# Kernel optimization log

Hardware: AMD Instinct MI355X
Metric: run time of the kernel (lower is better)

Reference implementation:

```python
import jax, jax.numpy as jnp
import numpy as np

# Dims: batch B, seq S, model dim D (= embedding_size = input_size of every block
# since hidden_size == embedding_size), sLSTM hidden H.
B, S, D, H = 8, 1024, 1024, 1024
NBLOCKS = 2
EPS = 1e-5  # nn.LayerNorm default


def _xavier(key, shape):
    fan_out, fan_in = shape
    lim = float(np.sqrt(6.0 / (fan_in + fan_out)))
    return jax.random.uniform(key, shape, jnp.float32, -lim, lim)


def setup_inputs() -> dict:
    key = jax.random.key(0)
    ks = jax.random.split(key, 1 + NBLOCKS * 4)
    inp = {"input_seq": jax.random.normal(ks[0], (B, S, D), jnp.float32)}
    for i in range(NBLOCKS):
        din = D  # every block has input_size == hidden_size == 1024
        k = ks[1 + 4 * i: 1 + 4 * (i + 1)]
        # fused gate weights, gate order [i, f, z, o]
        inp[f"W{i}"] = _xavier(k[0], (4 * H, din))      # input->gates
        inp[f"R{i}"] = _xavier(k[1], (4 * H, H))        # recurrent h->gates
        inp[f"b{i}"] = jnp.zeros((4 * H,), jnp.float32)
        inp[f"projW{i}"] = _xavier(k[2], (din, H))      # block output proj (xavier, zero bias per reset_parameters)
        inp[f"projb{i}"] = jnp.zeros((din,), jnp.float32)
        inp[f"gamma{i}"] = jnp.ones((din,), jnp.float32)   # LayerNorm weight
        inp[f"beta{i}"] = jnp.zeros((din,), jnp.float32)   # LayerNorm bias
    return inp


def _slstm(x, W, R, b):
    """Exponential-gated, log-stabilized sLSTM scan. x: (B,S,Din) -> (B,S,H)."""
    Hh = R.shape[1]
    Bn = x.shape[0]
    # precompute input contribution to all 4 gates: (B,S,4H) -> time-major (S,B,4H)
    xp = jnp.swapaxes(jnp.einsum('bsd,gd->bsg', x, W) + b, 0, 1)
    zeros = jnp.zeros((Bn, Hh), x.dtype)

    def step(carry, xpt):
        h, c, n, m = carry  # hidden, cell, normalizer, log-stabilizer
        pre = xpt + h @ R.T                       # (B,4H)
        i_pre, f_pre, z_pre, o_pre = jnp.split(pre, 4, axis=-1)
        m_new = jnp.maximum(f_pre + m, i_pre)     # stabilizer update
        i_g = jnp.exp(i_pre - m_new)              # stabilized exp input gate
        f_g = jnp.exp(f_pre + m - m_new)          # stabilized exp forget gate
        c_new = f_g * c + i_g * jnp.tanh(z_pre)
        n_new = f_g * n + i_g
        h_new = jax.nn.sigmoid(o_pre) * (c_new / n_new)
        return (h_new, c_new, n_new, m_new), h_new

    _, hs = jax.lax.scan(step, (zeros, zeros, zeros, zeros), xp)
    return jnp.swapaxes(hs, 0, 1)  # (B,S,H)


def _layernorm(x, g, bta):
    mu = jnp.mean(x, axis=-1, keepdims=True)
    var = jnp.var(x, axis=-1, keepdims=True)
    return (x - mu) * jax.lax.rsqrt(var + EPS) * g + bta


def reference(input_seq, W0, R0, b0, projW0, projb0, gamma0, beta0,
              W1, R1, b1, projW1, projb1, gamma1, beta1):
    x = input_seq
    for (W, R, b, pW, pb, g, bt) in (
            (W0, R0, b0, projW0, projb0, gamma0, beta0),
            (W1, R1, b1, projW1, projb1, gamma1, beta1)):
        hseq = _slstm(x, W, R, b)
        y = jax.nn.gelu(hseq @ pW.T + pb, approximate=False)  # GELU(proj(lstm_out))
        x = _layernorm(y + x, g, bt)                          # norm(out + residual); dropout=0
    return x
```

## Files before the change

### kernel.cpp

```cpp
#include <hip/hip_runtime.h>
#include <cstdint>
#include <cmath>

typedef unsigned short u16;
typedef unsigned long long u64;
typedef __attribute__((ext_vector_type(8))) short short8;
typedef __attribute__((ext_vector_type(4))) float f32x4;

#define SEQ 1024
#define HD 1024
#define GD 4096
#define NB 8
#define MROWS 8192

__device__ __forceinline__ u16 f2bf(float f) {
  union { float f; uint32_t u; } c; c.f = f;
  uint32_t u = c.u;
  uint32_t r = (u + 0x7fffu + ((u >> 16) & 1u)) >> 16;
  return (u16)r;
}
__device__ __forceinline__ float bf2f(u16 h) {
  union { uint32_t u; float f; } c; c.u = ((uint32_t)h) << 16;
  return c.f;
}

__global__ void k_tobf16(const float* __restrict__ in, u16* __restrict__ out, long n) {
  long i = ((long)blockIdx.x * 256L + threadIdx.x) * 4;
  long st = (long)gridDim.x * 1024L;
  for (; i < n; i += st) {
    float4 v = *(const float4*)(in + i);
    ushort4 o;
    o.x = f2bf(v.x); o.y = f2bf(v.y); o.z = f2bf(v.z); o.w = f2bf(v.w);
    *(ushort4*)(out + i) = o;
  }
}

template<int MODE>
__global__ __launch_bounds__(256, 1) void k_gemm(
    const u16* __restrict__ A, const u16* __restrict__ Bw,
    const float* __restrict__ bias, const float* __restrict__ res,
    u16* __restrict__ outb, float* __restrict__ outf, int N, int K)
{
  __shared__ u16 As[128][40];
  __shared__ u16 Bs[128][40];
  const int tid = threadIdx.x;
  const int wid = tid >> 6, lane = tid & 63;
  const int wm = wid >> 1, wn = wid & 1;
  const int r = lane & 15, q = lane >> 4;
  const long m0 = (long)blockIdx.y * 128, n0 = (long)blockIdx.x * 128;
  const int srow = tid >> 1, sseg = (tid & 1) * 16;

  f32x4 acc[4][4];
#pragma unroll
  for (int i = 0; i < 4; ++i)
#pragma unroll
    for (int j = 0; j < 4; ++j) acc[i][j] = (f32x4){0.f, 0.f, 0.f, 0.f};

  const u16* ag = A + (m0 + srow) * (long)K + sseg;
  const u16* bg = Bw + (n0 + srow) * (long)K + sseg;

  for (int k0 = 0; k0 < K; k0 += 32) {
    short8 av0 = *(const short8*)(ag + k0);
    short8 av1 = *(const short8*)(ag + k0 + 8);
    short8 bv0 = *(const short8*)(bg + k0);
    short8 bv1 = *(const short8*)(bg + k0 + 8);
    __syncthreads();
    *(short8*)&As[srow][sseg]     = av0;
    *(short8*)&As[srow][sseg + 8] = av1;
    *(short8*)&Bs[srow][sseg]     = bv0;
    *(short8*)&Bs[srow][sseg + 8] = bv1;
    __syncthreads();
    short8 bfr[4];
#pragma unroll
    for (int ni = 0; ni < 4; ++ni)
      bfr[ni] = *(const short8*)&Bs[wn * 64 + ni * 16 + r][q * 8];
#pragma unroll
    for (int mi = 0; mi < 4; ++mi) {
      short8 afr = *(const short8*)&As[wm * 64 + mi * 16 + r][q * 8];
#pragma unroll
      for (int ni = 0; ni < 4; ++ni)
        acc[mi][ni] = __builtin_amdgcn_mfma_f32_16x16x32_bf16(afr, bfr[ni], acc[mi][ni], 0, 0, 0);
    }
  }

#pragma unroll
  for (int mi = 0; mi < 4; ++mi)
#pragma unroll
    for (int ni = 0; ni < 4; ++ni) {
      long col = n0 + wn * 64 + ni * 16 + r;
      float bc = bias[col];
#pragma unroll
      for (int rr = 0; rr < 4; ++rr) {
        long row = m0 + wm * 64 + mi * 16 + q * 4 + rr;
        float v = acc[mi][ni][rr] + bc;
        if (MODE == 0) {
          long b = row >> 10, t = row & 1023;
          outb[((t * 8 + b) << 12) + col] = f2bf(v);
        } else {
          float ge = 0.5f * v * (1.0f + erff(v * 0.70710678118654752f));
          outf[row * N + col] = ge + res[row * N + col];
        }
      }
    }
}

__global__ __launch_bounds__(512, 1) void k_scan(
    const u16* __restrict__ xp, const u16* __restrict__ Rb,
    u16* __restrict__ hseq, u64* __restrict__ hx, int tagbase)
{
  __shared__ float Dred[2][8][128];
  __shared__ u16 xpf[4][4][32];
  __shared__ u16 hhist[2][32][32];

  const int tid = threadIdx.x;
  const int wgid = blockIdx.x;
  const int b = wgid & 7, c = wgid >> 3;
  const int w = tid >> 6, lane = tid & 63;
  const int r = lane & 15, q = lane >> 4;

  short8 wt[8][4];
#pragma unroll
  for (int j = 0; j < 8; ++j) {
    const int coll = j * 16 + r;
    const int g = coll >> 5, u = coll & 31;
    const u16* src = Rb + ((long)(g * HD + c * 32 + u)) * HD + w * 128 + q * 8;
#pragma unroll
    for (int s = 0; s < 4; ++s)
      wt[j][s] = *(const short8*)(src + s * 32);
  }

  if (w == 0 && lane < 32) {
    const int g = lane >> 3, o4 = (lane & 7) * 4;
#pragma unroll
    for (int t = 0; t < 2; ++t) {
      u64 v = *(const u64*)(xp + ((long)(t * 8 + b) << 12) + g * 1024 + c * 32 + o4);
      *(u64*)&xpf[t][g][o4] = v;
    }
  }
  __syncthreads();

  float c_s = 0.f, n_s = 0.f, m_s = 0.f;

  for (int i = 0; i < SEQ; ++i) {
    if (i > 0) {
      const unsigned tg = (unsigned)(tagbase + i - 1) & 0xffffu;
      const u64* src = hx + ((long)(b * 2 + ((i - 1) & 1)) << 9) + (w << 6) + lane;
      u64 hv;
#pragma unroll 1
      for (;;) {
        hv = __hip_atomic_load(src, __ATOMIC_RELAXED, __HIP_MEMORY_SCOPE_AGENT);
        if ((((unsigned)(hv >> 16)) & 0xffffu) == tg &&
            ((unsigned)(hv >> 48)) == tg) break;
      }
      unsigned pk = ((unsigned)hv & 0xffffu) | (((unsigned)(hv >> 32) & 0xffffu) << 16);

      f32x4 acc[8];
#pragma unroll
      for (int j = 0; j < 8; ++j) acc[j] = (f32x4){0.f, 0.f, 0.f, 0.f};
#pragma unroll
      for (int s = 0; s < 4; ++s) {
        union { unsigned x[4]; short8 v; } af;
#pragma unroll
        for (int m2 = 0; m2 < 4; ++m2)
          af.x[m2] = __shfl(pk, s * 16 + q * 4 + m2, 64);
#pragma unroll
        for (int j = 0; j < 8; ++j)
          acc[j] = __builtin_amdgcn_mfma_f32_16x16x32_bf16(af.v, wt[j][s], acc[j], 0, 0, 0);
      }
      if (q == 0) {
#pragma unroll
        for (int j = 0; j < 8; ++j)
          Dred[i & 1][w][j * 16 + r] = acc[j][0];
      }
    }
    __syncthreads();

    if (w == 7) {
      const int u = lane & 31;
      float pre[4];
#pragma unroll
      for (int g = 0; g < 4; ++g) {
        float s2 = bf2f(xpf[i & 3][g][u]);
        if (i > 0) {
#pragma unroll
          for (int w2 = 0; w2 < 8; ++w2) s2 += Dred[i & 1][w2][g * 32 + u];
        }
        pre[g] = s2;
      }
      float og = 1.f / (1.f + __expf(-pre[3]));
      float mn = fmaxf(pre[1] + m_s, pre[0]);
      float ig = __expf(pre[0] - mn);
      float fg = __expf(pre[1] + m_s - mn);
      float e2 = __expf(2.f * pre[2]);
      float th = 1.f - 2.f / (e2 + 1.f);
      c_s = fg * c_s + ig * th;
      n_s = fg * n_s + ig;
      m_s = mn;
      float h = og * (c_s / n_s);

      unsigned hu = (unsigned)f2bf(h);
      unsigned word = (((unsigned)(tagbase + i) & 0xffffu) << 16) | hu;
      unsigned wa = __shfl(word, (lane * 2) & 63, 64);
      unsigned wb = __shfl(word, (lane * 2 + 1) & 63, 64);
      if (lane < 16 && i < SEQ - 1) {
        u64 v64 = (u64)wa | ((u64)wb << 32);
        __hip_atomic_store(hx + ((long)(b * 2 + (i & 1)) << 9) + (c << 4) + lane,
                           v64, __ATOMIC_RELAXED, __HIP_MEMORY_SCOPE_AGENT);
      }
      if (lane < 32) hhist[(i >> 5) & 1][i & 31][lane] = (u16)hu;
    } else if (w == 0 && lane < 32 && i + 2 < SEQ) {
      const int g = lane >> 3, o4 = (lane & 7) * 4;
      u64 v = *(const u64*)(xp + ((long)((i + 2) * 8 + b) << 12) + g * 1024 + c * 32 + o4);
      *(u64*)&xpf[(i + 2) & 3][g][o4] = v;
    } else if (w == 6 && lane < 32 && i > 0 && (i & 31) == 0) {
      const int bank = ((i >> 5) & 1) ^ 1;
#pragma unroll
      for (int j = 0; j < 4; ++j) {
        short8 v = *(const short8*)&hhist[bank][lane][j * 8];
        *(short8*)(hseq + ((long)(b * SEQ + (i - 32 + lane))) * HD + c * 32 + j * 8) = v;
      }
    }
  }

  __syncthreads();

  if (w == 6 && lane < 32) {
#pragma unroll
    for (int j = 0; j < 4; ++j) {
      short8 v = *(const short8*)&hhist[1][lane][j * 8];
      *(short8*)(hseq + ((long)(b * SEQ + (SEQ - 32 + lane))) * HD + c * 32 + j * 8) = v;
    }
  }
}

__global__ __launch_bounds__(256, 1) void k_ln(
    const float* __restrict__ z, const float* __restrict__ gamma, const float* __restrict__ beta,
    float* __restrict__ xout, u16* __restrict__ xb)
{
  const int row = blockIdx.x, tid = threadIdx.x;
  const float4 v = *(const float4*)(z + (long)row * HD + tid * 4);
  float s = v.x + v.y + v.z + v.w;
  float s2 = v.x * v.x + v.y * v.y + v.z * v.z + v.w * v.w;
#pragma unroll
  for (int off = 32; off > 0; off >>= 1) {
    s += __shfl_down(s, off, 64);
    s2 += __shfl_down(s2, off, 64);
  }
  __shared__ float red[8];
  const int wid = tid >> 6, lane = tid & 63;
  if (lane == 0) { red[wid] = s; red[4 + wid] = s2; }
  __syncthreads();
  float su = red[0] + red[1] + red[2] + red[3];
  float sq = red[4] + red[5] + red[6] + red[7];
  float mu = su * (1.f / 1024.f);
  float var = sq * (1.f / 1024.f) - mu * mu;
  float rs = rsqrtf(var + 1e-5f);
  const float4 g  = *(const float4*)(gamma + tid * 4);
  const float4 bt = *(const float4*)(beta + tid * 4);
  float4 o;
  o.x = (v.x - mu) * rs * g.x + bt.x;
  o.y = (v.y - mu) * rs * g.y + bt.y;
  o.z = (v.z - mu) * rs * g.z + bt.z;
  o.w = (v.w - mu) * rs * g.w + bt.w;
  *(float4*)(xout + (long)row * HD + tid * 4) = o;
  ushort4 ob;
  ob.x = f2bf(o.x); ob.y = f2bf(o.y); ob.z = f2bf(o.z); ob.w = f2bf(o.w);
  *(ushort4*)(xb + (long)row * HD + tid * 4) = ob;
}

extern "C" void kernel_launch(void* const* d_in, const int* in_sizes, int n_in,
                              void* d_out, int out_size, void* d_ws, size_t ws_size,
                              hipStream_t stream)
{
  const float* input = (const float*)d_in[0];
  const float* W[2]  = { (const float*)d_in[1], (const float*)d_in[8] };
  const float* R[2]  = { (const float*)d_in[2], (const float*)d_in[9] };
  const float* bb[2] = { (const float*)d_in[3], (const float*)d_in[10] };
  const float* pW[2] = { (const float*)d_in[4], (const float*)d_in[11] };
  const float* pb[2] = { (const float*)d_in[5], (const float*)d_in[12] };
  const float* gm[2] = { (const float*)d_in[6], (const float*)d_in[13] };
  const float* bt[2] = { (const float*)d_in[7], (const float*)d_in[14] };
  float* out = (float*)d_out;

  char* p = (char*)d_ws;
  size_t off = 0;
  auto alloc = [&](size_t bytes) { char* q = p + off; off += (bytes + 255) & ~(size_t)255; return (void*)q; };
  u64* hx = (u64*)alloc(NB * 2 * 512 * 8);
  u16* xb     = (u16*)alloc((size_t)MROWS * HD * 2);
  u16* Wb[2]  = { (u16*)alloc((size_t)GD * HD * 2), (u16*)alloc((size_t)GD * HD * 2) };
  u16* Rbv[2] = { (u16*)alloc((size_t)GD * HD * 2), (u16*)alloc((size_t)GD * HD * 2) };
  u16* pWb[2] = { (u16*)alloc((size_t)HD * HD * 2), (u16*)alloc((size_t)HD * HD * 2) };
  u16* xpb    = (u16*)alloc((size_t)MROWS * GD * 2);
  u16* hs     = (u16*)alloc((size_t)MROWS * HD * 2);
  float* zb   = (float*)alloc((size_t)MROWS * HD * 4);
  float* x1   = (float*)alloc((size_t)MROWS * HD * 4);

  auto conv = [&](const float* src, u16* dst, long n) {
    int blocks = (int)((n / 4 + 255) / 256); if (blocks > 2048) blocks = 2048;
    k_tobf16<<<dim3(blocks), dim3(256), 0, stream>>>(src, dst, n);
  };
  conv(input, xb, (long)MROWS * HD);
  conv(W[0], Wb[0], (long)GD * HD);  conv(W[1], Wb[1], (long)GD * HD);
  conv(R[0], Rbv[0], (long)GD * HD); conv(R[1], Rbv[1], (long)GD * HD);
  conv(pW[0], pWb[0], (long)HD * HD); conv(pW[1], pWb[1], (long)HD * HD);

  hipMemsetAsync(hx, 0xAA, NB * 2 * 512 * 8, stream);

  for (int l = 0; l < 2; ++l) {
    k_gemm<0><<<dim3(GD / 128, MROWS / 128), 256, 0, stream>>>(
        xb, Wb[l], bb[l], nullptr, xpb, nullptr, GD, HD);
    k_scan<<<dim3(256), dim3(512), 0, stream>>>(xpb, Rbv[l], hs, hx, l * 1024);
    const float* resp = (l == 0) ? input : x1;
    k_gemm<1><<<dim3(HD / 128, MROWS / 128), 256, 0, stream>>>(
        hs, pWb[l], pb[l], resp, nullptr, zb, HD, HD);
    float* xo = (l == 0) ? x1 : out;
    k_ln<<<dim3(MROWS), dim3(256), 0, stream>>>(zb, gm[l], bt[l], xo, xb);
  }
}
```

Measured before the change: 4.719 ms.

## Repartition sLSTM scan so each wave owns 4 hidden units with full-K MFMA

```diff
diff --git a/kernel.cpp b/kernel.cpp
--- a/kernel.cpp
+++ b/kernel.cpp
@@ -106,45 +106,40 @@
 
 __global__ __launch_bounds__(512, 1) void k_scan(
     const u16* __restrict__ xp, const u16* __restrict__ Rb,
-    u16* __restrict__ hseq, u64* __restrict__ hx, int tagbase)
+    u16* __restrict__ hseq, uint32_t* __restrict__ hx, int tagbase)
 {
-  __shared__ float Dred[2][8][128];
-  __shared__ u16 xpf[4][4][32];
-  __shared__ u16 hhist[2][32][32];
+  __shared__ u16 hbuf[2][1024];
 
   const int tid = threadIdx.x;
   const int wgid = blockIdx.x;
   const int b = wgid & 7, c = wgid >> 3;
-  const int w = tid >> 6, lane = tid & 63;
-  const int r = lane & 15, q = lane >> 4;
-
-  short8 wt[8][4];
-#pragma unroll
-  for (int j = 0; j < 8; ++j) {
-    const int coll = j * 16 + r;
-    const int g = coll >> 5, u = coll & 31;
-    const u16* src = Rb + ((long)(g * HD + c * 32 + u)) * HD + w * 128 + q * 8;
-#pragma unroll
-    for (int s = 0; s < 4; ++s)
-      wt[j][s] = *(const short8*)(src + s * 32);
-  }
-
-  if (w == 0 && lane < 32) {
-    const int g = lane >> 3, o4 = (lane & 7) * 4;
-#pragma unroll
-    for (int t = 0; t < 2; ++t) {
-      u64 v = *(const u64*)(xp + ((long)(t * 8 + b) << 12) + g * 1024 + c * 32 + o4);
-      *(u64*)&xpf[t][g][o4] = v;
-    }
-  }
-  __syncthreads();
+  const int lane = tid & 63;
+  const int row = lane & 15, q = lane >> 4;
+  const int u_loc = row >> 2, g = row & 3;
+  const int unit0 = c * 32 + ((tid >> 6) << 2);
+
+  short8 wt[32];
+  {
+    const u16* src = Rb + ((long)(g * HD + unit0 + u_loc)) * HD + q * 8;
+#pragma unroll
+    for (int m = 0; m < 32; ++m)
+      wt[m] = *(const short8*)(src + m * 32);
+  }
+
+  const bool ldr = (q == 1 && row < 4);
+  u64 xq_cur = 0, xq_nxt = 0;
+  if (ldr) {
+    xq_cur = *(const u64*)(xp + ((long)(0 * 8 + b) << 12) + row * 1024 + unit0);
+    xq_nxt = *(const u64*)(xp + ((long)(1 * 8 + b) << 12) + row * 1024 + unit0);
+  }
 
   float c_s = 0.f, n_s = 0.f, m_s = 0.f;
+  const u64* hx64 = (const u64*)hx;
 
   for (int i = 0; i < SEQ; ++i) {
     if (i > 0) {
       const unsigned tg = (unsigned)(tagbase + i - 1) & 0xffffu;
-      const u64* src = hx + ((long)(b * 2 + ((i - 1) & 1)) << 9) + (w << 6) + lane;
+      const u64* src = hx64 + ((long)(b * 2 + ((i - 1) & 1)) << 9) + tid;
       u64 hv;
 #pragma unroll 1
       for (;;) {
@@ -152,84 +147,71 @@
         if ((((unsigned)(hv >> 16)) & 0xffffu) == tg &&
             ((unsigned)(hv >> 48)) == tg) break;
       }
-      unsigned pk = ((unsigned)hv & 0xffffu) | (((unsigned)(hv >> 32) & 0xffffu) << 16);
-
-      f32x4 acc[8];
-#pragma unroll
-      for (int j = 0; j < 8; ++j) acc[j] = (f32x4){0.f, 0.f, 0.f, 0.f};
-#pragma unroll
-      for (int s = 0; s < 4; ++s) {
-        union { unsigned x[4]; short8 v; } af;
-#pragma unroll
-        for (int m2 = 0; m2 < 4; ++m2)
-          af.x[m2] = __shfl(pk, s * 16 + q * 4 + m2, 64);
-#pragma unroll
-        for (int j = 0; j < 8; ++j)
-          acc[j] = __builtin_amdgcn_mfma_f32_16x16x32_bf16(af.v, wt[j][s], acc[j], 0, 0, 0);
+      unsigned pk = ((unsigned)hv & 0xffffu) | (((unsigned)(hv >> 32)) << 16);
+      *(uint32_t*)&hbuf[(i - 1) & 1][tid * 2] = pk;
+    }
+    __syncthreads();
+
+    float pre = 0.f;
+    if (i > 0) {
+      const u16* hb = hbuf[(i - 1) & 1];
+      f32x4 a0 = {0.f,0.f,0.f,0.f}, a1 = {0.f,0.f,0.f,0.f};
+      f32x4 a2 = {0.f,0.f,0.f,0.f}, a3 = {0.f,0.f,0.f,0.f};
+#pragma unroll
+      for (int m = 0; m < 32; m += 4) {
+        short8 v0 = *(const short8*)&hb[(m + 0) * 32 + q * 8];
+        short8 v1 = *(const short8*)&hb[(m + 1) * 32 + q * 8];
+        short8 v2 = *(const short8*)&hb[(m + 2) * 32 + q * 8];
+        short8 v3 = *(const short8*)&hb[(m + 3) * 32 + q * 8];
+        a0 = __builtin_amdgcn_mfma_f32_16x16x32_bf16(v0, wt[m + 0], a0, 0, 0, 0);
+        a1 = __builtin_amdgcn_mfma_f32_16x16x32_bf16(v1, wt[m + 1], a1, 0, 0, 0);
+        a2 = __builtin_amdgcn_mfma_f32_16x16x32_bf16(v2, wt[m + 2], a2, 0, 0, 0);
+        a3 = __builtin_amdgcn_mfma_f32_16x16x32_bf16(v3, wt[m + 3], a3, 0, 0, 0);
       }
-      if (q == 0) {
-#pragma unroll
-        for (int j = 0; j < 8; ++j)
-          Dred[i & 1][w][j * 16 + r] = acc[j][0];
-      }
-    }
-    __syncthreads();
-
-    if (w == 7) {
-      const int u = lane & 31;
-      float pre[4];
-#pragma unroll
-      for (int g = 0; g < 4; ++g) {
-        float s2 = bf2f(xpf[i & 3][g][u]);
-        if (i > 0) {
-#pragma unroll
-          for (int w2 = 0; w2 < 8; ++w2) s2 += Dred[i & 1][w2][g * 32 + u];
-        }
-        pre[g] = s2;
-      }
-      float og = 1.f / (1.f + __expf(-pre[3]));
-      float mn = fmaxf(pre[1] + m_s, pre[0]);
-      float ig = __expf(pre[0] - mn);
-      float fg = __expf(pre[1] + m_s - mn);
-      float e2 = __expf(2.f * pre[2]);
+      pre = (a0[0] + a1[0]) + (a2[0] + a3[0]);
+    }
+
+    {
+      u64 xv = __shfl(xq_cur, 16 + g, 64);
+      pre += bf2f((u16)(xv >> (u_loc * 16)));
+    }
+
+    float p1 = __shfl_down(pre, 1, 64);
+    float p2 = __shfl_down(pre, 2, 64);
+    float p3 = __shfl_down(pre, 3, 64);
+    float hval = 0.f;
+    if (q == 0 && (row & 3) == 0) {
+      float mn = fmaxf(p1 + m_s, pre);
+      float ig = __expf(pre - mn);
+      float fg = __expf(p1 + m_s - mn);
+      float e2 = __expf(2.f * p2);
       float th = 1.f - 2.f / (e2 + 1.f);
       c_s = fg * c_s + ig * th;
       n_s = fg * n_s + ig;
       m_s = mn;
-      float h = og * (c_s / n_s);
-
-      unsigned hu = (unsigned)f2bf(h);
-      unsigned word = (((unsigned)(tagbase + i) & 0xffffu) << 16) | hu;
-      unsigned wa = __shfl(word, (lane * 2) & 63, 64);
-      unsigned wb = __shfl(word, (lane * 2 + 1) & 63, 64);
-      if (lane < 16 && i < SEQ - 1) {
-        u64 v64 = (u64)wa | ((u64)wb << 32);
-        __hip_atomic_store(hx + ((long)(b * 2 + (i & 1)) << 9) + (c << 4) + lane,
-                           v64, __ATOMIC_RELAXED, __HIP_MEMORY_SCOPE_AGENT);
-      }
-      if (lane < 32) hhist[(i >> 5) & 1][i & 31][lane] = (u16)hu;
-    } else if (w == 0 && lane < 32 && i + 2 < SEQ) {
-      const int g = lane >> 3, o4 = (lane & 7) * 4;
-      u64 v = *(const u64*)(xp + ((long)((i + 2) * 8 + b) << 12) + g * 1024 + c * 32 + o4);
-      *(u64*)&xpf[(i + 2) & 3][g][o4] = v;
-    } else if (w == 6 && lane < 32 && i > 0 && (i & 31) == 0) {
-      const int bank = ((i >> 5) & 1) ^ 1;
-#pragma unroll
-      for (int j = 0; j < 4; ++j) {
-        short8 v = *(const short8*)&hhist[bank][lane][j * 8];
-        *(short8*)(hseq + ((long)(b * SEQ + (i - 32 + lane))) * HD + c * 32 + j * 8) = v;
-      }
-    }
-  }
-
-  __syncthreads();
-
-  if (w == 6 && lane < 32) {
-#pragma unroll
-    for (int j = 0; j < 4; ++j) {
-      short8 v = *(const short8*)&hhist[1][lane][j * 8];
-      *(short8*)(hseq + ((long)(b * SEQ + (SEQ - 32 + lane))) * HD + c * 32 + j * 8) = v;
-    }
+      float og = 1.f / (1.f + __expf(-p3));
+      hval = og * (c_s / n_s);
+    }
+    unsigned hu = (unsigned)f2bf(hval);
+    unsigned h0 = __shfl(hu, 0, 64), h1 = __shfl(hu, 4, 64);
+    unsigned h2 = __shfl(hu, 8, 64), h3 = __shfl(hu, 12, 64);
+
+    if (lane < 2 && i < SEQ - 1) {
+      const unsigned t16 = ((unsigned)(tagbase + i) & 0xffffu) << 16;
+      u64 v64 = (lane == 0)
+        ? ((u64)(t16 | h0) | ((u64)(t16 | h1) << 32))
+        : ((u64)(t16 | h2) | ((u64)(t16 | h3) << 32));
+      u64* dst = (u64*)hx + ((long)(b * 2 + (i & 1)) << 9) + (unit0 >> 1) + lane;
+      __hip_atomic_store(dst, v64, __ATOMIC_RELAXED, __HIP_MEMORY_SCOPE_AGENT);
+    }
+    if (lane == 2) {
+      u64 hp = (u64)(h0 | (h1 << 16)) | ((u64)(h2 | (h3 << 16)) << 32);
+      *(u64*)(hseq + ((long)(b * SEQ + i)) * HD + unit0) = hp;
+    }
+
+    xq_cur = xq_nxt;
+    if (ldr && i + 2 < SEQ)
+      xq_nxt = *(const u64*)(xp + ((long)((i + 2) * 8 + b) << 12) + row * 1024 + unit0);
   }
 }
 
@@ -285,7 +267,7 @@
   char* p = (char*)d_ws;
   size_t off = 0;
   auto alloc = [&](size_t bytes) { char* q = p + off; off += (bytes + 255) & ~(size_t)255; return (void*)q; };
-  u64* hx = (u64*)alloc(NB * 2 * 512 * 8);
+  uint32_t* hx = (uint32_t*)alloc(NB * 2 * HD * 4);
   u16* xb     = (u16*)alloc((size_t)MROWS * HD * 2);
   u16* Wb[2]  = { (u16*)alloc((size_t)GD * HD * 2), (u16*)alloc((size_t)GD * HD * 2) };
   u16* Rbv[2] = { (u16*)alloc((size_t)GD * HD * 2), (u16*)alloc((size_t)GD * HD * 2) };
@@ -304,7 +286,7 @@
   conv(R[0], Rbv[0], (long)GD * HD); conv(R[1], Rbv[1], (long)GD * HD);
   conv(pW[0], pWb[0], (long)HD * HD); conv(pW[1], pWb[1], (long)HD * HD);
 
-  hipMemsetAsync(hx, 0xAA, NB * 2 * 512 * 8, stream);
+  hipMemsetAsync(hx, 0xAA, NB * 2 * HD * 4, stream);
 
   for (int l = 0; l < 2; ++l) {
     k_gemm<0><<<dim3(GD / 128, MROWS / 128), 256, 0, stream>>>(
```

Result: faster. 4.009 ms (-15.0%).
